# Performance work log

Hardware: AMD Instinct MI355X
Metric: run time of the kernel (lower is better)

The kernel has to match this reference:

```python
import jax, jax.numpy as jnp
import numpy as np

B, N, C = 16, 1024, 768
H = 12
HD = C // H
MLP = 4 * C
EPS = 1e-5  # torch nn.LayerNorm default
LS_INIT = 1e-5


def _ln(x, g, b):
    mu = jnp.mean(x, axis=-1, keepdims=True)
    var = jnp.var(x, axis=-1, keepdims=True)
    return (x - mu) * jax.lax.rsqrt(var + EPS) * g + b


def setup_inputs() -> dict:
    key = jax.random.key(0)
    ks = jax.random.split(key, 8)
    s = 0.02
    return {
        "x": jax.random.normal(ks[0], (B, N, C), dtype=jnp.float32),
        "w_qkv": jax.random.normal(ks[1], (C, 3 * C), dtype=jnp.float32) * s,
        "w_proj": jax.random.normal(ks[2], (C, C), dtype=jnp.float32) * s,
        "b_proj": jnp.zeros((C,), jnp.float32),
        "ln1_g": jnp.ones((C,), jnp.float32),
        "ln1_b": jnp.zeros((C,), jnp.float32),
        "ln2_g": jnp.ones((C,), jnp.float32),
        "ln2_b": jnp.zeros((C,), jnp.float32),
        "ls1_g": jnp.full((C,), LS_INIT, jnp.float32),
        "ls2_g": jnp.full((C,), LS_INIT, jnp.float32),
        "w_fc1": jax.random.normal(ks[3], (C, MLP), dtype=jnp.float32) * s,
        "b_fc1": jnp.zeros((MLP,), jnp.float32),
        "w_fc2": jax.random.normal(ks[4], (MLP, C), dtype=jnp.float32) * s,
        "b_fc2": jnp.zeros((C,), jnp.float32),
    }


def reference(x, w_qkv, w_proj, b_proj, ln1_g, ln1_b, ln2_g, ln2_b,
              ls1_g, ls2_g, w_fc1, b_fc1, w_fc2, b_fc2):
    scale = HD ** -0.5
    # ---- attention branch (pre-norm) ----
    h = x
    y = _ln(x, ln1_g, ln1_b)
    qkv = (y @ w_qkv).reshape(B, N, 3, H, HD)
    q, k, v = (jnp.moveaxis(qkv, 2, 0)[i].transpose(0, 2, 1, 3) for i in range(3))  # [B,H,N,HD]
    attn = jnp.einsum("bhnd,bhmd->bhnm", q * scale, k)
    attn = attn - jnp.max(attn, axis=-1, keepdims=True)  # explicit max-subtract as in source
    attn = jax.nn.softmax(attn, axis=-1)
    o = jnp.einsum("bhnm,bhmd->bhnd", attn, v).transpose(0, 2, 1, 3).reshape(B, N, C)
    o = o @ w_proj + b_proj
    x = h + o * ls1_g  # LayerScale (fp32)
    # ---- MLP branch ----
    h = x
    y = _ln(x, ln2_g, ln2_b)
    y = jax.nn.gelu(y @ w_fc1 + b_fc1, approximate=False)
    y = y @ w_fc2 + b_fc2
    x = h + y * ls2_g
    return x  # weights=None since vis=False
```

## Files before the change

kernel.cpp:

```cpp
#include <hip/hip_runtime.h>
#include <cstdint>
#include <cstddef>

typedef __bf16 bf16;
typedef __bf16 bf16x4 __attribute__((ext_vector_type(4)));
typedef __bf16 bf16x8 __attribute__((ext_vector_type(8)));
typedef _Float16 f16;
typedef _Float16 f16x2 __attribute__((ext_vector_type(2)));
typedef _Float16 f16x4 __attribute__((ext_vector_type(4)));
typedef _Float16 f16x8 __attribute__((ext_vector_type(8)));
typedef float  f32x4  __attribute__((ext_vector_type(4)));
typedef float  f32x16 __attribute__((ext_vector_type(16)));
typedef int    i32x4  __attribute__((ext_vector_type(4)));
typedef int    i32x8  __attribute__((ext_vector_type(8)));
typedef unsigned char u8;

#define B_   16
#define N_   1024
#define C_   768
#define H_   12
#define HD_  64
#define M_   (B_*N_)
#define MLP_ 3072
#define QKVN 2304
#define WSCALE 64.0f
#define WINV  (1.0f/64.0f)
#define CEXP_ 0.18033688f

__device__ __forceinline__ void gll16(const void* g, void* l) {
  __builtin_amdgcn_global_load_lds((const __attribute__((address_space(1))) void*)g,
                                   (__attribute__((address_space(3))) void*)l,
                                   16, 0, 0);
}

template <int N>
__device__ __forceinline__ void wait_vm() {
  if constexpr (N == 0)      asm volatile("s_waitcnt vmcnt(0)" ::: "memory");
  else if constexpr (N == 3) asm volatile("s_waitcnt vmcnt(3)" ::: "memory");
  else                       asm volatile("s_waitcnt vmcnt(4)" ::: "memory");
}

__device__ __forceinline__ float fast_exp2(float x) { return __builtin_amdgcn_exp2f(x); }
__device__ __forceinline__ float fast_rcp(float x)  { return __builtin_amdgcn_rcpf(x); }

__device__ __forceinline__ f16x2 cvt_pk_f16(float a, float b) {
  return __builtin_bit_cast(f16x2, __builtin_amdgcn_cvt_pkrtz(a, b));
}

__device__ __forceinline__ u8 to_fp8(float a) {
  return (u8)(__builtin_amdgcn_cvt_pk_fp8_f32(a, a, 0, false) & 0xff);
}
__device__ __forceinline__ int to_fp8x4(float v0, float v1, float v2, float v3) {
  int p = __builtin_amdgcn_cvt_pk_fp8_f32(v0, v1, 0, false);
  p = __builtin_amdgcn_cvt_pk_fp8_f32(v2, v3, p, true);
  return p;
}

#define T_QKV  1728
#define T_PROJ 2304
#define T_FC1  4608
#define T_FC2  6912
#define T_ALL  6912

__device__ __forceinline__ void tc_tile(const float* __restrict__ w, u8* __restrict__ wt,
                                        int K, int N, int t, int tid) {
  __shared__ float tile[32][33];
  int tiles_n = N >> 5;
  int n0 = (t % tiles_n) * 32, k0 = (t / tiles_n) * 32;
  int tx = tid & 31, ty = tid >> 5;
  #pragma unroll
  for (int i = 0; i < 32; i += 8)
    tile[ty + i][tx] = w[(size_t)(k0 + ty + i) * N + n0 + tx];
  __syncthreads();
  #pragma unroll
  for (int i = 0; i < 32; i += 8)
    wt[(size_t)(n0 + ty + i) * K + k0 + tx] = to_fp8(tile[tx][ty + i] * WSCALE);
}

__global__ __launch_bounds__(256)
void prep_kernel(const float* __restrict__ x,
                 const float* __restrict__ w_qkv, const float* __restrict__ w_proj,
                 const float* __restrict__ w_fc1, const float* __restrict__ w_fc2,
                 const float* __restrict__ g, const float* __restrict__ bta,
                 u8* __restrict__ wqkvT, u8* __restrict__ wprojT,
                 u8* __restrict__ wfc1T, u8* __restrict__ wfc2T,
                 u8* __restrict__ y) {
  int bid = blockIdx.x, tid = threadIdx.x;
  if (bid < T_ALL) {
    if (bid < T_QKV)       tc_tile(w_qkv,  wqkvT,  C_,   QKVN, bid,          tid);
    else if (bid < T_PROJ) tc_tile(w_proj, wprojT, C_,   C_,   bid - T_QKV,  tid);
    else if (bid < T_FC1)  tc_tile(w_fc1,  wfc1T,  C_,   MLP_, bid - T_PROJ, tid);
    else                   tc_tile(w_fc2,  wfc2T,  MLP_, C_,   bid - T_FC1,  tid);
    return;
  }
  int row = bid - T_ALL;
  const float* xr = x + (size_t)row * C_;
  float v0 = xr[tid], v1 = xr[tid + 256], v2 = xr[tid + 512];
  float s  = v0 + v1 + v2;
  float sq = v0 * v0 + v1 * v1 + v2 * v2;
  #pragma unroll
  for (int off = 32; off > 0; off >>= 1) {
    s  += __shfl_xor(s,  off);
    sq += __shfl_xor(sq, off);
  }
  __shared__ float red[8];
  int wave = tid >> 6, lane = tid & 63;
  if (lane == 0) { red[wave] = s; red[4 + wave] = sq; }
  __syncthreads();
  s  = red[0] + red[1] + red[2] + red[3];
  sq = red[4] + red[5] + red[6] + red[7];
  float mean = s * (1.0f / C_);
  float var  = sq * (1.0f / C_) - mean * mean;
  float rstd = rsqrtf(var + 1e-5f);
  u8* yr = y + (size_t)row * C_;
  yr[tid]       = to_fp8((v0 - mean) * rstd * g[tid]       + bta[tid]);
  yr[tid + 256] = to_fp8((v1 - mean) * rstd * g[tid + 256] + bta[tid + 256]);
  yr[tid + 512] = to_fp8((v2 - mean) * rstd * g[tid + 512] + bta[tid + 512]);
}

__global__ __launch_bounds__(256)
void ln_cast_kernel(const float* __restrict__ x, const float* __restrict__ g,
                    const float* __restrict__ bta, u8* __restrict__ y) {
  int row = blockIdx.x;
  int tid = threadIdx.x;
  const float* xr = x + (size_t)row * C_;
  float v0 = xr[tid], v1 = xr[tid + 256], v2 = xr[tid + 512];
  float s  = v0 + v1 + v2;
  float sq = v0 * v0 + v1 * v1 + v2 * v2;
  #pragma unroll
  for (int off = 32; off > 0; off >>= 1) {
    s  += __shfl_xor(s,  off);
    sq += __shfl_xor(sq, off);
  }
  __shared__ float red[8];
  int wave = tid >> 6, lane = tid & 63;
  if (lane == 0) { red[wave] = s; red[4 + wave] = sq; }
  __syncthreads();
  s  = red[0] + red[1] + red[2] + red[3];
  sq = red[4] + red[5] + red[6] + red[7];
  float mean = s * (1.0f / C_);
  float var  = sq * (1.0f / C_) - mean * mean;
  float rstd = rsqrtf(var + 1e-5f);
  u8* yr = y + (size_t)row * C_;
  yr[tid]       = to_fp8((v0 - mean) * rstd * g[tid]       + bta[tid]);
  yr[tid + 256] = to_fp8((v1 - mean) * rstd * g[tid + 256] + bta[tid + 256]);
  yr[tid + 512] = to_fp8((v2 - mean) * rstd * g[tid + 512] + bta[tid + 512]);
}

template <int EPI, int BN_>
__global__ __launch_bounds__(512, 2)
void gemm_bt(const u8* __restrict__ A, const u8* __restrict__ Bt,
             void* __restrict__ outp, const float* __restrict__ bias,
             const float* __restrict__ ls, const float* __restrict__ resid,
             f16* __restrict__ vt_out,
             int M, int N, int K, int nb) {
  constexpr int BM = 256, BK = 64;
  constexpr int NJ  = BN_ / 128;
  constexpr int NBL = BN_ / 128;
  constexpr int TL  = 2 + NBL;
  __shared__ __align__(16) u8 As[3][BM * BK];
  __shared__ __align__(16) u8 Bs[3][BN_ * BK];
  int tid  = threadIdx.x;
  int lane = tid & 63, wave = tid >> 6;
  int h32 = lane >> 5, r5 = lane & 31;
  int bid = blockIdx.x;
  int xcd = bid & 7, seq = bid >> 3;
  int mi = xcd + 8 * (seq / nb), ni = seq % nb;
  int m0 = mi * BM, n0 = ni * BN_;
  int wm = (wave >> 2) * 128, wn = (wave & 3) * (BN_ / 4);

  int iters = K >> 6;
  int skew  = (ni * iters) / nb;

  const u8* ag[2]; const u8* bg[NBL];
  #pragma unroll
  for (int s = 0; s < 2; s++) {
    int u = tid + s * 512;
    int r = u >> 2, g = (u & 3) ^ ((r >> 1) & 3);
    ag[s] = A + (size_t)(m0 + r) * K + g * 16;
  }
  #pragma unroll
  for (int s = 0; s < NBL; s++) {
    int u = tid + s * 512;
    int r = u >> 2, g = (u & 3) ^ ((r >> 1) & 3);
    bg[s] = Bt + (size_t)(n0 + r) * K + g * 16;
  }
  int sw  = (r5 >> 1) & 3;
  int go0 = ((2 * h32 + 0) ^ sw) * 16;
  int go1 = ((2 * h32 + 1) ^ sw) * 16;

  f32x16 acc[4][NJ];
  #pragma unroll
  for (int i = 0; i < 4; i++)
    #pragma unroll
    for (int j = 0; j < NJ; j++)
      #pragma unroll
      for (int rg = 0; rg < 16; rg++) acc[i][j][rg] = 0.f;

  int k0 = skew;
  int k1 = (skew + 1 == iters) ? 0 : skew + 1;
  {
    int kn = k0 * BK;
    gll16(ag[0] + kn, &As[0][0] + tid * 16);
    gll16(ag[1] + kn, &As[0][0] + 8192 + tid * 16);
    gll16(bg[0] + kn, &Bs[0][0] + tid * 16);
    if constexpr (NBL == 2) gll16(bg[1] + kn, &Bs[0][0] + 8192 + tid * 16);
    kn = k1 * BK;
    gll16(ag[0] + kn, &As[1][0] + tid * 16);
    gll16(ag[1] + kn, &As[1][0] + 8192 + tid * 16);
    gll16(bg[0] + kn, &Bs[1][0] + tid * 16);
    if constexpr (NBL == 2) gll16(bg[1] + kn, &Bs[1][0] + 8192 + tid * 16);
  }
  wait_vm<TL>();
  __builtin_amdgcn_s_barrier();
  int kiss = (k1 + 1 == iters) ? 0 : k1 + 1;

  int buf_c = 0;
  for (int t = 0; t < iters; t++) {
    if (t + 2 < iters) {
      int bi = (buf_c == 0) ? 2 : buf_c - 1;
      int kn = kiss * BK;
      gll16(ag[0] + kn, &As[bi][0] + tid * 16);
      gll16(ag[1] + kn, &As[bi][0] + 8192 + tid * 16);
      gll16(bg[0] + kn, &Bs[bi][0] + tid * 16);
      if constexpr (NBL == 2) gll16(bg[1] + kn, &Bs[bi][0] + 8192 + tid * 16);
      kiss = (kiss + 1 == iters) ? 0 : kiss + 1;
    }
    i32x8 af[4], bfr[NJ];
    #pragma unroll
    for (int i = 0; i < 4; i++) {
      const u8* pa = &As[buf_c][0] + (wm + i * 32 + r5) * 64;
      i32x4 lo = *(const i32x4*)(pa + go0);
      i32x4 hi = *(const i32x4*)(pa + go1);
      af[i] = __builtin_shufflevector(lo, hi, 0, 1, 2, 3, 4, 5, 6, 7);
    }
    #pragma unroll
    for (int j = 0; j < NJ; j++) {
      const u8* pb = &Bs[buf_c][0] + (wn + j * 32 + r5) * 64;
      i32x4 lo = *(const i32x4*)(pb + go0);
      i32x4 hi = *(const i32x4*)(pb + go1);
      bfr[j] = __builtin_shufflevector(lo, hi, 0, 1, 2, 3, 4, 5, 6, 7);
    }
    __builtin_amdgcn_s_setprio(1);
    #pragma unroll
    for (int i = 0; i < 4; i++)
      #pragma unroll
      for (int j = 0; j < NJ; j++)
        acc[i][j] = __builtin_amdgcn_mfma_scale_f32_32x32x64_f8f6f4(
            af[i], bfr[j], acc[i][j], 0, 0, 0, 0x7f7f7f7f, 0, 0x7f7f7f7f);
    __builtin_amdgcn_s_setprio(0);
    if (t + 1 < iters) {
      if (t + 2 < iters) wait_vm<TL>();
      else               wait_vm<0>();
      __builtin_amdgcn_s_barrier();
    }
    buf_c = (buf_c == 2) ? 0 : buf_c + 1;
  }

  #pragma unroll
  for (int i = 0; i < 4; i++) {
    int rowb = m0 + wm + i * 32 + h32 * 4;
    #pragma unroll
    for (int j = 0; j < NJ; j++) {
      int col = n0 + wn + j * 32 + r5;
      float bias_c = (EPI == 0) ? 0.f : bias[col];
      float ls_c   = (EPI == 1 || EPI == 3) ? ls[col] : 0.f;
      float gz_v = -2.45546696f * WINV;
      float gz_b = -2.45546696f * bias_c;
      if constexpr (EPI == 0) {
        float sc0 = (col < C_) ? (WINV * CEXP_) : WINV;
        bool isv = (n0 + wn + j * 32) >= 2 * C_;
        #pragma unroll
        for (int g = 0; g < 4; g++) {
          f16x4 vv;
          #pragma unroll
          for (int rr = 0; rr < 4; rr++) {
            float v = acc[i][j][4 * g + rr];
            int row = rowb + rr + 8 * g;
            ((bf16*)outp)[(size_t)row * N + col] = (bf16)(v * sc0);
            vv[rr] = (f16)(v * WINV);
          }
          if (isv) {
            int row0 = rowb + 8 * g;
            int bb = row0 >> 10, nn = row0 & 1023;
            int hh = (col - 2 * C_) >> 6, dd = (col - 2 * C_) & 63;
            *(f16x4*)(vt_out + ((size_t)(bb * H_ + hh) * HD_ + dd) * N_ + nn) = vv;
          }
        }
      } else {
        #pragma unroll
        for (int rg = 0; rg < 16; rg++) {
          float v = acc[i][j][rg];
          int row = rowb + (rg & 3) + 8 * (rg >> 2);
          size_t idx = (size_t)row * N + col;
          if constexpr (EPI == 1) {
            float t = fmaf(v, WINV, bias_c);
            ((float*)outp)[idx] = fmaf(t, ls_c, resid[idx]);
          } else if constexpr (EPI == 2) {
            float t  = fmaf(v, WINV, bias_c);
            float zn = fmaf(v, gz_v, gz_b);
            float gv = t * fast_rcp(1.0f + fast_exp2(zn));
            ((u8*)outp)[idx] = to_fp8(gv);
          } else {
            float t = fmaf(v, WINV, bias_c);
            ((float*)outp)[idx] = fmaf(t, ls_c, resid[idx]);
          }
        }
      }
    }
  }
}

__global__ __launch_bounds__(256)
void attn_kernel(const bf16* __restrict__ qkv, const f16* __restrict__ vt,
                 u8* __restrict__ o) {
  constexpr int KSTR = 72;
  constexpr int VSTR = 136;
  __shared__ __align__(16) bf16 Ks[128 * KSTR];
  __shared__ __align__(16) f16  Vs[HD_ * VSTR];

  int tid = threadIdx.x, lane = tid & 63, wave = tid >> 6;
  int quad = lane >> 4, l16 = lane & 15;
  int bid = blockIdx.x;
  int xcd = bid & 7, seq = bid >> 3;
  int bh = xcd + 8 * (seq >> 3);
  int b = bh / H_, h = bh % H_;
  int qt = seq & 7;
  int q0 = qt * 128;

  bf16x8 qf[2][2];
  #pragma unroll
  for (int i = 0; i < 2; i++)
    #pragma unroll
    for (int kk = 0; kk < 2; kk++)
      qf[i][kk] = *(const bf16x8*)(qkv + (size_t)(b * N_ + q0 + wave * 32 + i * 16 + l16) * QKVN
                                   + h * HD_ + kk * 32 + quad * 8);

  const f32x4 fz = {0.f, 0.f, 0.f, 0.f};
  f32x4 oacc[2][4];
  float l_run[2];
  #pragma unroll
  for (int i = 0; i < 2; i++) {
    #pragma unroll
    for (int jd = 0; jd < 4; jd++) oacc[i][jd] = fz;
    l_run[i] = 0.f;
  }

  const bf16* kbase = qkv + (size_t)(b * N_) * QKVN + C_ + h * HD_;
  const f16*  vbase = vt + (size_t)bh * HD_ * N_;

  int kr[4], kc[4], vr[4], vc[4];
  #pragma unroll
  for (int u = 0; u < 4; u++) {
    int L = tid + u * 256;
    kr[u] = L >> 3;  kc[u] = (L & 7) * 8;
    vr[u] = L >> 4;  vc[u] = (L & 15) * 8;
  }

  bf16x8 kreg[4]; f16x8 vreg[4];
  {
    int kv = qt * 128;
    #pragma unroll
    for (int u = 0; u < 4; u++) {
      kreg[u] = *(const bf16x8*)(kbase + (size_t)(kv + kr[u]) * QKVN + kc[u]);
      vreg[u] = *(const f16x8*)(vbase + (size_t)vr[u] * N_ + kv + vc[u]);
    }
  }

  for (int t = 0; t < 8; t++) {
    __syncthreads();
    #pragma unroll
    for (int u = 0; u < 4; u++) {
      *(bf16x8*)(Ks + kr[u] * KSTR + kc[u]) = kreg[u];
      *(f16x8*)(Vs + vr[u] * VSTR + vc[u])  = vreg[u];
    }
    __syncthreads();

    if (t + 1 < 8) {
      int kv = ((t + 1 + qt) & 7) * 128;
      #pragma unroll
      for (int u = 0; u < 4; u++) {
        kreg[u] = *(const bf16x8*)(kbase + (size_t)(kv + kr[u]) * QKVN + kc[u]);
        vreg[u] = *(const f16x8*)(vbase + (size_t)vr[u] * N_ + kv + vc[u]);
      }
    }

    f32x4 sv[2][8];
    #pragma unroll
    for (int i = 0; i < 2; i++)
      #pragma unroll
      for (int kf = 0; kf < 8; kf++) sv[i][kf] = fz;
    #pragma unroll
    for (int kk = 0; kk < 2; kk++) {
      #pragma unroll
      for (int kf = 0; kf < 8; kf++) {
        bf16x8 kb = *(const bf16x8*)(Ks + (kf * 16 + l16) * KSTR + kk * 32 + quad * 8);
        sv[0][kf] = __builtin_amdgcn_mfma_f32_16x16x32_bf16(kb, qf[0][kk], sv[0][kf], 0, 0, 0);
        sv[1][kf] = __builtin_amdgcn_mfma_f32_16x16x32_bf16(kb, qf[1][kk], sv[1][kf], 0, 0, 0);
      }
    }

    f16x4 pb[2][8];
    #pragma unroll
    for (int i = 0; i < 2; i++) {
      f16x2 rs2 = {(f16)0.f, (f16)0.f};
      #pragma unroll
      for (int kf = 0; kf < 8; kf++) {
        float p0 = fast_exp2(sv[i][kf][0]);
        float p1 = fast_exp2(sv[i][kf][1]);
        float p2 = fast_exp2(sv[i][kf][2]);
        float p3 = fast_exp2(sv[i][kf][3]);
        f16x2 h0 = cvt_pk_f16(p0, p1);
        f16x2 h1 = cvt_pk_f16(p2, p3);
        pb[i][kf] = __builtin_shufflevector(h0, h1, 0, 1, 2, 3);
        rs2 += h0;
        rs2 += h1;
      }
      float rs = (float)rs2[0] + (float)rs2[1];
      rs += __shfl_xor(rs, 16);
      rs += __shfl_xor(rs, 32);
      l_run[i] += rs;
    }

    #pragma unroll
    for (int kb2 = 0; kb2 < 4; kb2++) {
      f16x8 pb32_0 = __builtin_shufflevector(pb[0][2 * kb2], pb[0][2 * kb2 + 1],
                                             0, 1, 2, 3, 4, 5, 6, 7);
      f16x8 pb32_1 = __builtin_shufflevector(pb[1][2 * kb2], pb[1][2 * kb2 + 1],
                                             0, 1, 2, 3, 4, 5, 6, 7);
      #pragma unroll
      for (int jd = 0; jd < 4; jd++) {
        const f16* vp = Vs + (jd * 16 + l16) * VSTR + kb2 * 32 + quad * 4;
        f16x4 v0 = *(const f16x4*)(vp);
        f16x4 v1 = *(const f16x4*)(vp + 16);
        f16x8 va8 = __builtin_shufflevector(v0, v1, 0, 1, 2, 3, 4, 5, 6, 7);
        oacc[0][jd] = __builtin_amdgcn_mfma_f32_16x16x32_f16(va8, pb32_0, oacc[0][jd], 0, 0, 0);
        oacc[1][jd] = __builtin_amdgcn_mfma_f32_16x16x32_f16(va8, pb32_1, oacc[1][jd], 0, 0, 0);
      }
    }
  }

  #pragma unroll
  for (int i = 0; i < 2; i++) {
    float inv = fast_rcp(l_run[i]);
    int n = q0 + wave * 32 + i * 16 + l16;
    #pragma unroll
    for (int jd = 0; jd < 4; jd++) {
      int p = to_fp8x4(oacc[i][jd][0] * inv, oacc[i][jd][1] * inv,
                       oacc[i][jd][2] * inv, oacc[i][jd][3] * inv);
      *(int*)(o + (size_t)(b * N_ + n) * C_ + h * HD_ + jd * 16 + quad * 4) = p;
    }
  }
}

#define WQKVT_OFF  0u
#define WPROJT_OFF 1769472u
#define WFC1T_OFF  2359296u
#define WFC2T_OFF  4718592u
#define Y_OFF      7077888u
#define QKV_OFF    19660800u
#define VT_OFF     95158272u
#define O_OFF      120324096u
#define X1_OFF     132907008u
#define WS_NEEDED  183238656u

extern "C" void kernel_launch(void* const* d_in, const int* in_sizes, int n_in,
                              void* d_out, int out_size, void* d_ws, size_t ws_size,
                              hipStream_t stream) {
  if (ws_size < (size_t)WS_NEEDED) return;

  const float* x      = (const float*)d_in[0];
  const float* w_qkv  = (const float*)d_in[1];
  const float* w_proj = (const float*)d_in[2];
  const float* b_proj = (const float*)d_in[3];
  const float* ln1_g  = (const float*)d_in[4];
  const float* ln1_b  = (const float*)d_in[5];
  const float* ln2_g  = (const float*)d_in[6];
  const float* ln2_b  = (const float*)d_in[7];
  const float* ls1_g  = (const float*)d_in[8];
  const float* ls2_g  = (const float*)d_in[9];
  const float* w_fc1  = (const float*)d_in[10];
  const float* b_fc1  = (const float*)d_in[11];
  const float* w_fc2  = (const float*)d_in[12];
  const float* b_fc2  = (const float*)d_in[13];

  char* ws = (char*)d_ws;
  u8*    wqkvT  = (u8*)(ws + WQKVT_OFF);
  u8*    wprojT = (u8*)(ws + WPROJT_OFF);
  u8*    wfc1T  = (u8*)(ws + WFC1T_OFF);
  u8*    wfc2T  = (u8*)(ws + WFC2T_OFF);
  u8*    y      = (u8*)(ws + Y_OFF);
  bf16*  qkv    = (bf16*)(ws + QKV_OFF);
  u8*    hbuf   = (u8*)(ws + QKV_OFF);
  f16*   vt     = (f16*)(ws + VT_OFF);
  u8*    o      = (u8*)(ws + O_OFF);
  float* x1     = (float*)(ws + X1_OFF);
  float* out    = (float*)d_out;

  prep_kernel<<<T_ALL + M_, 256, 0, stream>>>(
      x, w_qkv, w_proj, w_fc1, w_fc2, ln1_g, ln1_b,
      wqkvT, wprojT, wfc1T, wfc2T, y);

  gemm_bt<0, 256><<<(M_ / 256) * (QKVN / 256), 512, 0, stream>>>(
      y, wqkvT, qkv, nullptr, nullptr, nullptr, vt, M_, QKVN, C_, QKVN / 256);

  attn_kernel<<<(N_ / 128) * B_ * H_, 256, 0, stream>>>(qkv, vt, o);

  gemm_bt<1, 128><<<(M_ / 256) * (C_ / 128), 512, 0, stream>>>(
      o, wprojT, x1, b_proj, ls1_g, x, nullptr, M_, C_, C_, C_ / 128);

  ln_cast_kernel<<<M_, 256, 0, stream>>>(x1, ln2_g, ln2_b, y);

  gemm_bt<2, 256><<<(M_ / 256) * (MLP_ / 256), 512, 0, stream>>>(
      y, wfc1T, hbuf, b_fc1, nullptr, nullptr, nullptr, M_, MLP_, C_, MLP_ / 256);

  gemm_bt<3, 128><<<(M_ / 256) * (C_ / 128), 512, 0, stream>>>(
      hbuf, wfc2T, out, b_fc2, ls2_g, x1, nullptr, M_, C_, MLP_, C_ / 128);
}
```

Measured before the change: 448.1 us.

## Double-buffer K tiles in LDS and read V directly from global in attention

Attention keeps two LDS buffers for K tiles and prefetches K two steps ahead, which cuts the loop to one barrier per step instead of two. V is no longer staged in LDS; each wave loads its V fragments straight from the transposed V tensor in global memory (likely served by L2) just before the PV MFMAs. The PV section also raises wave priority via s_setprio. This removes LDS traffic and a barrier per step, at the cost of uncoalesced global V reads that every wave repeats and added latency in the MFMA chain.

```diff
diff --git a/kernel.cpp b/kernel.cpp
--- a/kernel.cpp
+++ b/kernel.cpp
@@ -315,9 +315,7 @@
 void attn_kernel(const bf16* __restrict__ qkv, const f16* __restrict__ vt,
                  u8* __restrict__ o) {
   constexpr int KSTR = 72;
-  constexpr int VSTR = 136;
-  __shared__ __align__(16) bf16 Ks[128 * KSTR];
-  __shared__ __align__(16) f16  Vs[HD_ * VSTR];
+  __shared__ __align__(16) bf16 Ks[2][128 * KSTR];
 
   int tid = threadIdx.x, lane = tid & 63, wave = tid >> 6;
   int quad = lane >> 4, l16 = lane & 15;
@@ -349,40 +347,41 @@
   const bf16* kbase = qkv + (size_t)(b * N_) * QKVN + C_ + h * HD_;
   const f16*  vbase = vt + (size_t)bh * HD_ * N_;
 
-  int kr[4], kc[4], vr[4], vc[4];
+  int kr[4], kc[4];
   #pragma unroll
   for (int u = 0; u < 4; u++) {
     int L = tid + u * 256;
     kr[u] = L >> 3;  kc[u] = (L & 7) * 8;
-    vr[u] = L >> 4;  vc[u] = (L & 15) * 8;
-  }
-
-  bf16x8 kreg[4]; f16x8 vreg[4];
+  }
+
+  bf16x8 kreg[4];
   {
     int kv = qt * 128;
     #pragma unroll
-    for (int u = 0; u < 4; u++) {
+    for (int u = 0; u < 4; u++)
       kreg[u] = *(const bf16x8*)(kbase + (size_t)(kv + kr[u]) * QKVN + kc[u]);
-      vreg[u] = *(const f16x8*)(vbase + (size_t)vr[u] * N_ + kv + vc[u]);
-    }
-  }
+    #pragma unroll
+    for (int u = 0; u < 4; u++)
+      *(bf16x8*)(&Ks[0][0] + kr[u] * KSTR + kc[u]) = kreg[u];
+    kv = ((1 + qt) & 7) * 128;
+    #pragma unroll
+    for (int u = 0; u < 4; u++)
+      kreg[u] = *(const bf16x8*)(kbase + (size_t)(kv + kr[u]) * QKVN + kc[u]);
+  }
+  __syncthreads();
 
   for (int t = 0; t < 8; t++) {
-    __syncthreads();
-    #pragma unroll
-    for (int u = 0; u < 4; u++) {
-      *(bf16x8*)(Ks + kr[u] * KSTR + kc[u]) = kreg[u];
-      *(f16x8*)(Vs + vr[u] * VSTR + vc[u])  = vreg[u];
-    }
-    __syncthreads();
-
+    int cur = t & 1;
     if (t + 1 < 8) {
-      int kv = ((t + 1 + qt) & 7) * 128;
-      #pragma unroll
-      for (int u = 0; u < 4; u++) {
+      #pragma unroll
+      for (int u = 0; u < 4; u++)
+        *(bf16x8*)(&Ks[cur ^ 1][0] + kr[u] * KSTR + kc[u]) = kreg[u];
+    }
+    if (t + 2 < 8) {
+      int kv = ((t + 2 + qt) & 7) * 128;
+      #pragma unroll
+      for (int u = 0; u < 4; u++)
         kreg[u] = *(const bf16x8*)(kbase + (size_t)(kv + kr[u]) * QKVN + kc[u]);
-        vreg[u] = *(const f16x8*)(vbase + (size_t)vr[u] * N_ + kv + vc[u]);
-      }
     }
 
     f32x4 sv[2][8];
@@ -394,7 +393,7 @@
     for (int kk = 0; kk < 2; kk++) {
       #pragma unroll
       for (int kf = 0; kf < 8; kf++) {
-        bf16x8 kb = *(const bf16x8*)(Ks + (kf * 16 + l16) * KSTR + kk * 32 + quad * 8);
+        bf16x8 kb = *(const bf16x8*)(&Ks[cur][0] + (kf * 16 + l16) * KSTR + kk * 32 + quad * 8);
         sv[0][kf] = __builtin_amdgcn_mfma_f32_16x16x32_bf16(kb, qf[0][kk], sv[0][kf], 0, 0, 0);
         sv[1][kf] = __builtin_amdgcn_mfma_f32_16x16x32_bf16(kb, qf[1][kk], sv[1][kf], 0, 0, 0);
       }
@@ -422,22 +421,31 @@
       l_run[i] += rs;
     }
 
+    int kvc = ((t + qt) & 7) * 128;
+    __builtin_amdgcn_s_setprio(1);
     #pragma unroll
     for (int kb2 = 0; kb2 < 4; kb2++) {
+      f16x8 va8[4];
+      #pragma unroll
+      for (int jd = 0; jd < 4; jd++) {
+        const f16* vp = vbase + (size_t)(jd * 16 + l16) * N_ + kvc + kb2 * 32 + quad * 4;
+        f16x4 v0 = *(const f16x4*)(vp);
+        f16x4 v1 = *(const f16x4*)(vp + 16);
+        va8[jd] = __builtin_shufflevector(v0, v1, 0, 1, 2, 3, 4, 5, 6, 7);
+      }
       f16x8 pb32_0 = __builtin_shufflevector(pb[0][2 * kb2], pb[0][2 * kb2 + 1],
                                              0, 1, 2, 3, 4, 5, 6, 7);
       f16x8 pb32_1 = __builtin_shufflevector(pb[1][2 * kb2], pb[1][2 * kb2 + 1],
                                              0, 1, 2, 3, 4, 5, 6, 7);
       #pragma unroll
       for (int jd = 0; jd < 4; jd++) {
-        const f16* vp = Vs + (jd * 16 + l16) * VSTR + kb2 * 32 + quad * 4;
-        f16x4 v0 = *(const f16x4*)(vp);
-        f16x4 v1 = *(const f16x4*)(vp + 16);
-        f16x8 va8 = __builtin_shufflevector(v0, v1, 0, 1, 2, 3, 4, 5, 6, 7);
-        oacc[0][jd] = __builtin_amdgcn_mfma_f32_16x16x32_f16(va8, pb32_0, oacc[0][jd], 0, 0, 0);
-        oacc[1][jd] = __builtin_amdgcn_mfma_f32_16x16x32_f16(va8, pb32_1, oacc[1][jd], 0, 0, 0);
+        oacc[0][jd] = __builtin_amdgcn_mfma_f32_16x16x32_f16(va8[jd], pb32_0, oacc[0][jd], 0, 0, 0);
+        oacc[1][jd] = __builtin_amdgcn_mfma_f32_16x16x32_f16(va8[jd], pb32_1, oacc[1][jd], 0, 0, 0);
       }
     }
+    __builtin_amdgcn_s_setprio(0);
+
+    if (t + 1 < 8) __syncthreads();
   }
 
   #pragma unroll
```

After: 571.3 us. 27.5% more time.
